# Performance work log

Hardware: AMD Instinct MI355X
Metric: run time of the kernel (lower is better)

Reference implementation:

```python
import jax, jax.numpy as jnp
import numpy as np

DIM = 192
NUM_HEADS = 6
WS = (7, 7, 7)
N_TOK = WS[0] * WS[1] * WS[2]  # 343
TABLE_SIZE = (2 * WS[0] - 1) * (2 * WS[1] - 1) * (2 * WS[2] - 1)  # 2197


def _relative_position_index():
    # faithful replication of the torch buffer construction (incl. its strides)
    coords = np.stack(np.meshgrid(np.arange(WS[0]), np.arange(WS[1]), np.arange(WS[2]), indexing='ij'))
    flat = coords.reshape(3, -1)                     # [3, N]
    rel = flat[:, :, None] - flat[:, None, :]        # [3, N, N]
    rel = rel.transpose(1, 2, 0).astype(np.int64)    # [N, N, 3]
    rel[..., 0] += WS[0] - 1
    rel[..., 1] += WS[1] - 1
    rel[..., 2] += WS[2] - 1
    rel[..., 0] *= 3 * WS[1] - 1  # = 20 (source uses window_size[1] here)
    rel[..., 1] *= 2 * WS[1] - 1  # = 13
    return rel.sum(-1)            # [N, N]


def setup_inputs() -> dict:
    key = jax.random.key(0)
    ks = jax.random.split(key, 10)
    B_, nW = 256, 64
    x1 = jax.random.normal(ks[0], (B_, N_TOK, DIM), dtype=jnp.float32)
    x2 = jax.random.normal(ks[1], (B_, N_TOK, DIM), dtype=jnp.float32)
    mask = jax.random.normal(ks[2], (nW, N_TOK, N_TOK), dtype=jnp.float32)
    table = 0.02 * jax.random.normal(ks[3], (TABLE_SIZE, NUM_HEADS), dtype=jnp.float32)
    s = DIM ** -0.5
    q_w = s * jax.random.normal(ks[4], (DIM, DIM), dtype=jnp.float32)
    q_b = jnp.zeros((DIM,), jnp.float32)
    kv_w = s * jax.random.normal(ks[5], (2 * DIM, DIM), dtype=jnp.float32)
    kv_b = jnp.zeros((2 * DIM,), jnp.float32)
    proj_w = s * jax.random.normal(ks[6], (DIM, DIM), dtype=jnp.float32)
    proj_b = jnp.zeros((DIM,), jnp.float32)
    rel_idx = jnp.asarray(_relative_position_index(), dtype=jnp.int32)
    return {"x1": x1, "x2": x2, "mask": mask, "table": table,
            "q_w": q_w, "q_b": q_b, "kv_w": kv_w, "kv_b": kv_b,
            "proj_w": proj_w, "proj_b": proj_b, "rel_idx": rel_idx}


def reference(x1, x2, mask, table, q_w, q_b, kv_w, kv_b, proj_w, proj_b, rel_idx):
    B_, N, C = x1.shape
    H = NUM_HEADS
    hd = C // H
    scale = hd ** -0.5
    # q from x1, k/v from x2 (isfusion cross-attention path)
    q = (x1 @ q_w.T + q_b).reshape(B_, N, H, hd).transpose(0, 2, 1, 3) * scale  # [B,H,N,hd]
    kv = (x2 @ kv_w.T + kv_b).reshape(B_, N, 2, H, hd).transpose(2, 0, 3, 1, 4)  # [2,B,H,N,hd]
    k, v = kv[0], kv[1]
    attn = jnp.einsum('bhnd,bhmd->bhnm', q, k)  # [B,H,N,N]
    # relative position bias gather -> [H,N,N]
    bias = table[rel_idx.reshape(-1)].reshape(N, N, H).transpose(2, 0, 1)
    attn = attn + bias[None]
    # shifted-window mask add
    nW = mask.shape[0]
    attn = (attn.reshape(B_ // nW, nW, H, N, N) + mask[None, :, None]).reshape(B_, H, N, N)
    attn = jax.nn.softmax(attn, axis=-1)
    out = jnp.einsum('bhnm,bhmd->bnhd', attn, v).reshape(B_, N, C)
    return out @ proj_w.T + proj_b
```

## Files before the change

kernel.cpp:

```cpp
#include <hip/hip_runtime.h>

typedef __attribute__((ext_vector_type(8))) short short8;
typedef __attribute__((ext_vector_type(4))) float f32x4;
typedef __attribute__((ext_vector_type(16))) float f32x16;
typedef __attribute__((ext_vector_type(4))) unsigned short us4;
typedef __attribute__((ext_vector_type(2))) unsigned int u32x2;

#define NTOK 343
#define BMP 352
#define LOG2E 1.4426950408889634f
#define FPLANE 11264
#define WPITCH 200

#define OFF_QG   0u
#define OFF_KG   33718272u
#define OFF_VT   68321280u
#define OFF_AO   102924288u
#define OFF_WB   136642560u

__device__ __forceinline__ unsigned short f2bf(float f) {
  union { float f; unsigned u; } v; v.f = f;
  unsigned r = v.u + 0x7FFFu + ((v.u >> 16) & 1u);
  return (unsigned short)(r >> 16);
}

__device__ __forceinline__ float bf2f(unsigned short b) {
  union { unsigned u; float f; } v; v.u = ((unsigned)b) << 16;
  return v.f;
}

__device__ __forceinline__ short8 ld8(const unsigned short* p) {
  return *reinterpret_cast<const short8*>(p);
}

__device__ __forceinline__ float fexp2(float x) {
  float r; asm("v_exp_f32 %0, %1" : "=v"(r) : "v"(x)); return r;
}

__device__ __forceinline__ unsigned cvtpk(float a, float b) {
  unsigned r; asm("v_cvt_pk_bf16_f32 %0, %1, %2" : "=v"(r) : "v"(a), "v"(b)); return r;
}

__device__ __forceinline__ void plswap(unsigned &a, unsigned &b) {
  asm("v_permlane32_swap_b32 %0, %1" : "+v"(a), "+v"(b));
}

__device__ __forceinline__ f32x16 mfma32(short8 a, short8 b, f32x16 c) {
  return __builtin_amdgcn_mfma_f32_32x32x16_bf16(a, b, c, 0, 0, 0);
}

__device__ __forceinline__ f32x4 mfma16(short8 a, short8 b, f32x4 c) {
  return __builtin_amdgcn_mfma_f32_16x16x32_bf16(a, b, c, 0, 0, 0);
}

union frag_u { unsigned u[4]; short8 s8; };

__device__ __forceinline__ short8 cvt8f(const float* p) {
  f32x4 a = *reinterpret_cast<const f32x4*>(p);
  f32x4 b = *reinterpret_cast<const f32x4*>(p + 4);
  frag_u f;
  f.u[0] = cvtpk(a[0], a[1]); f.u[1] = cvtpk(a[2], a[3]);
  f.u[2] = cvtpk(b[0], b[1]); f.u[3] = cvtpk(b[2], b[3]);
  return f.s8;
}

__global__ __launch_bounds__(256) void precompute(
    const float* __restrict__ mask, const float* __restrict__ table,
    const int* __restrict__ rel_idx,
    const float* __restrict__ qw, const float* __restrict__ kvw, const float* __restrict__ pw,
    unsigned short* __restrict__ wq_bf, unsigned short* __restrict__ wkv_bf,
    unsigned short* __restrict__ wp_bf,
    unsigned short* __restrict__ bias_bf, unsigned short* __restrict__ mask_bf,
    unsigned short* __restrict__ v_frag)
{
  const int idx = blockIdx.x * 256 + threadIdx.x;
  if (idx < 36864) {
    const int wi = idx;
    const float* src; unsigned short* dst; int i;
    if (wi < 9216)       { src = qw;  dst = wq_bf;  i = wi; }
    else if (wi < 27648) { src = kvw; dst = wkv_bf; i = wi - 9216; }
    else                 { src = pw;  dst = wp_bf;  i = wi - 27648; }
    f32x4 v = *reinterpret_cast<const f32x4*>(src + i * 4);
    us4 o; o[0] = f2bf(v[0]); o[1] = f2bf(v[1]); o[2] = f2bf(v[2]); o[3] = f2bf(v[3]);
    *reinterpret_cast<us4*>(dst + i * 4) = o;
  } else if (idx < 1968640) {
    const int mi = idx - 36864;
    const int row = mi / 88, q = mi - row * 88;
    const int j0 = q * 4;
    unsigned short* dst = mask_bf + row * BMP + j0;
    if (q < 85) {
      const float* src = mask + row * NTOK + j0;
      us4 o; o[0] = f2bf(LOG2E * src[0]); o[1] = f2bf(LOG2E * src[1]);
      o[2] = f2bf(LOG2E * src[2]); o[3] = f2bf(LOG2E * src[3]);
      *reinterpret_cast<us4*>(dst) = o;
    } else {
      us4 o;
      #pragma unroll
      for (int i = 0; i < 4; ++i) {
        const int col = j0 + i;
        o[i] = (col < NTOK) ? f2bf(LOG2E * mask[row * NTOK + col]) : (unsigned short)0;
      }
      *reinterpret_cast<us4*>(dst) = o;
    }
  } else if (idx < 2086289) {
    const int i = idx - 1968640;
    const int ri = rel_idx[i] * 6;
    const int rrow = i / NTOK, j = i - rrow * NTOK;
    unsigned short* dst = bias_bf + rrow * BMP + j;
    #pragma unroll
    for (int h = 0; h < 6; ++h) dst[h * (NTOK * BMP)] = f2bf(LOG2E * table[ri + h]);
  } else if (idx < 2088347) {
    const int p = idx - 2086289;
    unsigned short* dst = bias_bf + p * BMP + NTOK;
    #pragma unroll
    for (int c = 0; c < 9; ++c) dst[c] = 0;
  } else if (idx < 2284955) {
    const int i = idx - 2088347;
    const int bh = i >> 7, c = i & 127;
    short8 z = (short8){0,0,0,0,0,0,0,0};
    *reinterpret_cast<short8*>(v_frag + bh * FPLANE + 10240 + c * 8) = z;
  }
}

__global__ __launch_bounds__(256) void proj(
    const float* __restrict__ x1f, const float* __restrict__ x2f,
    const unsigned short* __restrict__ wq_bf, const unsigned short* __restrict__ wkv_bf,
    const float* __restrict__ qb, const float* __restrict__ kvb,
    unsigned short* __restrict__ q_g, unsigned short* __restrict__ k_g,
    unsigned short* __restrict__ v_frag)
{
  __shared__ __align__(16) unsigned short wLds[192 * WPITCH];

  const int tid = threadIdx.x;
  const int wv = tid >> 6, lane = tid & 63, lg = lane >> 4, lr = lane & 15;
  const int path = blockIdx.y;
  const int b = blockIdx.x & 255, seg = blockIdx.x >> 8;
  const int n0 = seg * 128 + wv * 32;

  const float* X = (path == 0) ? x1f : x2f;
  const unsigned short* Wsrc = (path == 0) ? wq_bf : (path == 1 ? wkv_bf : wkv_bf + 36864);

  #pragma unroll
  for (int i = 0; i < 18; ++i) {
    const int c = i * 256 + tid;
    const int row = c / 24, c8 = c - row * 24;
    *reinterpret_cast<short8*>(&wLds[row * WPITCH + c8 * 8]) = ld8(Wsrc + row * 192 + c8 * 8);
  }
  __syncthreads();

  const int rowbase = b * NTOK;
  const int nA = n0 + lr, nB = n0 + 16 + lr;
  const float* xr0 = X + (rowbase + (nA < NTOK ? nA : NTOK - 1)) * 192 + lg * 8;
  const float* xr1 = X + (rowbase + (nB < NTOK ? nB : NTOK - 1)) * 192 + lg * 8;

  short8 ax[2][6];
  #pragma unroll
  for (int kk = 0; kk < 6; ++kk) {
    ax[0][kk] = cvt8f(xr0 + kk * 32);
    ax[1][kk] = cvt8f(xr1 + kk * 32);
  }

  f32x4 acc[2][12];
  #pragma unroll
  for (int i = 0; i < 2; ++i)
    #pragma unroll
    for (int j = 0; j < 12; ++j) acc[i][j] = (f32x4){0.f, 0.f, 0.f, 0.f};

  if (path < 2) {
    #pragma unroll
    for (int kk = 0; kk < 6; ++kk) {
      const int k0 = kk * 32 + lg * 8;
      #pragma unroll
      for (int ct = 0; ct < 12; ++ct) {
        const short8 wf = *reinterpret_cast<const short8*>(&wLds[(ct * 16 + lr) * WPITCH + k0]);
        acc[0][ct] = mfma16(wf, ax[0][kk], acc[0][ct]);
        acc[1][ct] = mfma16(wf, ax[1][kk], acc[1][ct]);
      }
    }
    if (path == 0) {
      const float qs = 0.17677669529663687f * LOG2E;
      #pragma unroll
      for (int tt = 0; tt < 2; ++tt) {
        const int n = n0 + tt * 16 + lr;
        if (n < NTOK) {
          unsigned short* ob = q_g + (b * 6 * NTOK + n) * 32;
          #pragma unroll
          for (int ct = 0; ct < 12; ++ct) {
            const f32x4 bb = *reinterpret_cast<const f32x4*>(qb + ct * 16 + lg * 4);
            u32x2 pk;
            pk[0] = cvtpk((acc[tt][ct][0] + bb[0]) * qs, (acc[tt][ct][1] + bb[1]) * qs);
            pk[1] = cvtpk((acc[tt][ct][2] + bb[2]) * qs, (acc[tt][ct][3] + bb[3]) * qs);
            *reinterpret_cast<u32x2*>(ob + (ct >> 1) * (NTOK * 32) + (ct & 1) * 16 + lg * 4) = pk;
          }
        }
      }
    } else {
      #pragma unroll
      for (int tt = 0; tt < 2; ++tt) {
        const int n = n0 + tt * 16 + lr;
        if (n < 352) {
          unsigned short* ob = k_g + b * 6 * FPLANE + (n >> 5) * 1024
                               + ((lg >> 1) * 32 + (n & 31)) * 8 + (lg & 1) * 4;
          #pragma unroll
          for (int ct = 0; ct < 12; ++ct) {
            const f32x4 bb = *reinterpret_cast<const f32x4*>(kvb + ct * 16 + lg * 4);
            u32x2 pk;
            pk[0] = cvtpk(acc[tt][ct][0] + bb[0], acc[tt][ct][1] + bb[1]);
            pk[1] = cvtpk(acc[tt][ct][2] + bb[2], acc[tt][ct][3] + bb[3]);
            *reinterpret_cast<u32x2*>(ob + (ct >> 1) * FPLANE + (ct & 1) * 512) = pk;
          }
        }
      }
    }
  } else {
    #pragma unroll
    for (int kk = 0; kk < 6; ++kk) {
      const int k0 = kk * 32 + lg * 8;
      #pragma unroll
      for (int ct = 0; ct < 12; ++ct) {
        const short8 wf = *reinterpret_cast<const short8*>(&wLds[(ct * 16 + lr) * WPITCH + k0]);
        acc[0][ct] = mfma16(ax[0][kk], wf, acc[0][ct]);
        acc[1][ct] = mfma16(ax[1][kk], wf, acc[1][ct]);
      }
    }
    float bs[12];
    #pragma unroll
    for (int ct = 0; ct < 12; ++ct) bs[ct] = kvb[192 + ct * 16 + lr];
    #pragma unroll
    for (int tt = 0; tt < 2; ++tt) {
      const int nb = n0 + tt * 16 + lg * 4;
      if (nb < 352) {
        unsigned short* vb = v_frag + b * 6 * FPLANE + (nb >> 5) * 1024
                             + ((nb >> 4) & 1) * 512 + ((nb >> 3) & 1) * 256 + (nb & 7);
        #pragma unroll
        for (int ct = 0; ct < 12; ++ct) {
          const int d = (ct & 1) * 16 + lr;
          u32x2 pk;
          pk[0] = cvtpk(acc[tt][ct][0] + bs[ct], acc[tt][ct][1] + bs[ct]);
          pk[1] = cvtpk(acc[tt][ct][2] + bs[ct], acc[tt][ct][3] + bs[ct]);
          *reinterpret_cast<u32x2*>(vb + (ct >> 1) * FPLANE + d * 8) = pk;
        }
      }
    }
  }
}

__global__ __launch_bounds__(256, 3) void attn(
    const unsigned short* __restrict__ q_g, const unsigned short* __restrict__ k_g,
    const unsigned short* __restrict__ v_frag, const unsigned short* __restrict__ bias_bf,
    const unsigned short* __restrict__ mask_bf, unsigned short* __restrict__ attn_out)
{
  __shared__ __align__(16) unsigned short kvlds[2][FPLANE];

  const int tid = threadIdx.x;
  const int wv = tid >> 6, lane = tid & 63;
  const int l31 = lane & 31, hi = lane >> 5;
  const int s0 = blockIdx.x;
  const int xcd = s0 & 7, ii = s0 >> 3;
  const int g = xcd * 48 + (ii >> 2), mem = ii & 3;
  const int h = g >> 6, w = g & 63;
  const int b = mem * 64 + w;
  const int bid = b * 6 + h;

  const unsigned short* qp = q_g + bid * (NTOK * 32);
  const unsigned short* kpf = k_g + bid * FPLANE;
  const unsigned short* vpf = v_frag + bid * FPLANE;
  const unsigned short* bias_h = bias_bf + h * (NTOK * BMP);
  const unsigned short* mask_w = mask_bf + w * (NTOK * BMP);

  #pragma unroll
  for (int j = 0; j < 6; ++j) {
    const int c = j * 256 + tid;
    if (c < 1408) {
      *reinterpret_cast<short8*>(&kvlds[0][c * 8]) = ld8(kpf + c * 8);
      *reinterpret_cast<short8*>(&kvlds[1][c * 8]) = ld8(vpf + c * 8);
    }
  }
  __syncthreads();

  for (int qt = wv; qt < 11; qt += 4) {
    const int qq = qt * 32 + l31;
    const int qrc = qq < NTOK ? qq : NTOK - 1;
    const short8 qf0 = ld8(qp + qrc * 32 + hi * 8);
    const short8 qf1 = ld8(qp + qrc * 32 + 16 + hi * 8);
    const unsigned short* bmb = bias_h + qrc * BMP + hi * 4;
    const unsigned short* bmm = mask_w + qrc * BMP + hi * 4;

    f32x16 O;
    #pragma unroll
    for (int r = 0; r < 16; ++r) O[r] = 0.f;
    f32x4 sacc = (f32x4){0.f, 0.f, 0.f, 0.f};

    us4 nb[4], nm[4];
    #pragma unroll
    for (int gg = 0; gg < 4; ++gg) {
      nb[gg] = *reinterpret_cast<const us4*>(bmb + gg * 8);
      nm[gg] = *reinterpret_cast<const us4*>(bmm + gg * 8);
    }

    #pragma unroll
    for (int kt = 0; kt < 11; ++kt) {
      us4 cb[4], cm[4];
      #pragma unroll
      for (int gg = 0; gg < 4; ++gg) { cb[gg] = nb[gg]; cm[gg] = nm[gg]; }
      if (kt < 10) {
        const int kn = (kt + 1) * 32;
        #pragma unroll
        for (int gg = 0; gg < 4; ++gg) {
          nb[gg] = *reinterpret_cast<const us4*>(bmb + kn + gg * 8);
          nm[gg] = *reinterpret_cast<const us4*>(bmm + kn + gg * 8);
        }
      }

      const short8 kf0 = ld8(&kvlds[0][kt * 1024 + lane * 8]);
      const short8 kf1 = ld8(&kvlds[0][kt * 1024 + 512 + lane * 8]);
      f32x16 sv;
      #pragma unroll
      for (int r = 0; r < 16; ++r) sv[r] = 0.f;
      __builtin_amdgcn_s_setprio(1);
      sv = mfma32(kf0, qf0, sv);
      sv = mfma32(kf1, qf1, sv);
      __builtin_amdgcn_s_setprio(0);

      float p[16];
      #pragma unroll
      for (int gg = 0; gg < 4; ++gg) {
        #pragma unroll
        for (int j = 0; j < 4; ++j) {
          float v = sv[gg * 4 + j] + (bf2f(cb[gg][j]) + bf2f(cm[gg][j]));
          if (kt == 10 && (gg * 8 + hi * 4 + j) >= 23) v = -3.0e38f;
          p[gg * 4 + j] = fexp2(v);
        }
      }
      #pragma unroll
      for (int j = 0; j < 4; ++j)
        sacc[j] += (p[j] + p[4 + j]) + (p[8 + j] + p[12 + j]);

      unsigned c01 = cvtpk(p[0], p[1]),   c23 = cvtpk(p[2], p[3]);
      unsigned c45 = cvtpk(p[4], p[5]),   c67 = cvtpk(p[6], p[7]);
      unsigned d01 = cvtpk(p[8], p[9]),   d23 = cvtpk(p[10], p[11]);
      unsigned d45 = cvtpk(p[12], p[13]), d67 = cvtpk(p[14], p[15]);
      plswap(c01, c45); plswap(c23, c67);
      plswap(d01, d45); plswap(d23, d67);
      frag_u P0, P1;
      P0.u[0] = c01; P0.u[1] = c23; P0.u[2] = c45; P0.u[3] = c67;
      P1.u[0] = d01; P1.u[1] = d23; P1.u[2] = d45; P1.u[3] = d67;

      const short8 vf0 = ld8(&kvlds[1][kt * 1024 + lane * 8]);
      const short8 vf1 = ld8(&kvlds[1][kt * 1024 + 512 + lane * 8]);
      __builtin_amdgcn_s_setprio(1);
      O = mfma32(vf0, P0.s8, O);
      O = mfma32(vf1, P1.s8, O);
      __builtin_amdgcn_s_setprio(0);
    }

    float sum = (sacc[0] + sacc[1]) + (sacc[2] + sacc[3]);
    sum += __shfl_xor(sum, 32);
    const float inv = 1.0f / sum;
    if (qq < NTOK) {
      unsigned short* op = attn_out + (b * NTOK + qq) * 192 + h * 32;
      #pragma unroll
      for (int gg = 0; gg < 4; ++gg) {
        us4 ov;
        #pragma unroll
        for (int j = 0; j < 4; ++j) ov[j] = f2bf(O[gg * 4 + j] * inv);
        *reinterpret_cast<us4*>(op + gg * 8 + hi * 4) = ov;
      }
    }
  }
}

__global__ __launch_bounds__(256) void proj_out(
    const unsigned short* __restrict__ a_in, const unsigned short* __restrict__ wp_bf,
    const float* __restrict__ pb, float* __restrict__ out)
{
  __shared__ __align__(16) unsigned short wLds[192 * WPITCH];

  const int tid = threadIdx.x;
  const int wv = tid >> 6, lane = tid & 63, lg = lane >> 4, lr = lane & 15;
  const int t0 = blockIdx.x * 128 + wv * 32;

  #pragma unroll
  for (int i = 0; i < 18; ++i) {
    const int c = i * 256 + tid;
    const int row = c / 24, c8 = c - row * 24;
    *reinterpret_cast<short8*>(&wLds[row * WPITCH + c8 * 8]) = ld8(wp_bf + row * 192 + c8 * 8);
  }
  __syncthreads();

  const unsigned short* xr0 = a_in + (t0 + lr) * 192 + lg * 8;
  const unsigned short* xr1 = xr0 + 16 * 192;

  short8 ax[2][6];
  #pragma unroll
  for (int kk = 0; kk < 6; ++kk) {
    ax[0][kk] = ld8(xr0 + kk * 32);
    ax[1][kk] = ld8(xr1 + kk * 32);
  }

  f32x4 acc[2][12];
  #pragma unroll
  for (int i = 0; i < 2; ++i)
    #pragma unroll
    for (int j = 0; j < 12; ++j) acc[i][j] = (f32x4){0.f, 0.f, 0.f, 0.f};

  #pragma unroll
  for (int kk = 0; kk < 6; ++kk) {
    const int k0 = kk * 32 + lg * 8;
    #pragma unroll
    for (int ct = 0; ct < 12; ++ct) {
      const short8 wf = *reinterpret_cast<const short8*>(&wLds[(ct * 16 + lr) * WPITCH + k0]);
      acc[0][ct] = mfma16(wf, ax[0][kk], acc[0][ct]);
      acc[1][ct] = mfma16(wf, ax[1][kk], acc[1][ct]);
    }
  }

  #pragma unroll
  for (int tt = 0; tt < 2; ++tt) {
    const int t = t0 + tt * 16 + lr;
    float* op = out + t * 192 + lg * 4;
    #pragma unroll
    for (int ct = 0; ct < 12; ++ct) {
      const f32x4 bb = *reinterpret_cast<const f32x4*>(pb + ct * 16 + lg * 4);
      f32x4 ov;
      #pragma unroll
      for (int r = 0; r < 4; ++r) ov[r] = acc[tt][ct][r] + bb[r];
      *reinterpret_cast<f32x4*>(op + ct * 16) = ov;
    }
  }
}

extern "C" void kernel_launch(void* const* d_in, const int* in_sizes, int n_in,
                              void* d_out, int out_size, void* d_ws, size_t ws_size,
                              hipStream_t stream) {
  const float* x1    = (const float*)d_in[0];
  const float* x2    = (const float*)d_in[1];
  const float* mask  = (const float*)d_in[2];
  const float* table = (const float*)d_in[3];
  const float* qw    = (const float*)d_in[4];
  const float* qb    = (const float*)d_in[5];
  const float* kvw   = (const float*)d_in[6];
  const float* kvb   = (const float*)d_in[7];
  const float* pw    = (const float*)d_in[8];
  const float* pb    = (const float*)d_in[9];
  const int* rel_idx = (const int*)d_in[10];

  char* ws = (char*)d_ws;
  char* outc = (char*)d_out;
  unsigned short* q_g     = (unsigned short*)(ws + OFF_QG);
  unsigned short* k_g     = (unsigned short*)(ws + OFF_KG);
  unsigned short* v_frag  = (unsigned short*)(ws + OFF_VT);
  unsigned short* a_o     = (unsigned short*)(ws + OFF_AO);
  unsigned short* wq_bf   = (unsigned short*)(ws + OFF_WB);
  unsigned short* wkv_bf  = wq_bf + 36864;
  unsigned short* wp_bf   = wkv_bf + 73728;
  unsigned short* bias_bf = (unsigned short*)(outc + 33718272);
  unsigned short* mask_bf = (unsigned short*)(outc + 35167104);

  hipLaunchKernelGGL(precompute, dim3(8926), dim3(256), 0, stream,
                     mask, table, rel_idx, qw, kvw, pw,
                     wq_bf, wkv_bf, wp_bf, bias_bf, mask_bf, v_frag);
  hipLaunchKernelGGL(proj, dim3(768, 3), dim3(256), 0, stream,
                     x1, x2, wq_bf, wkv_bf, qb, kvb, q_g, k_g, v_frag);
  hipLaunchKernelGGL(attn, dim3(1536), dim3(256), 0, stream,
                     q_g, k_g, v_frag, bias_bf, mask_bf, a_o);
  hipLaunchKernelGGL(proj_out, dim3(686), dim3(256), 0, stream,
                     a_o, wp_bf, pb, (float*)d_out);
}
```

Before: 218.5 us.

## Use 512-thread attention blocks and store bias/mask in fp32

The attention kernel now runs 8 waves per block instead of 4. Each wave handles at most two of the 11 query tiles, which shortens the longest per-wave path. The precomputed relative-position bias and window mask are stored as fp32 instead of bf16, which removes the bf16-to-fp32 unpacking in the inner loop. The trade-off is twice the bias/mask memory traffic and more register pressure under launch_bounds(512,4), and the 11 tiles now spread unevenly across the 8 waves.

```diff
diff --git a/kernel.cpp b/kernel.cpp
--- a/kernel.cpp
+++ b/kernel.cpp
@@ -22,11 +22,6 @@
   union { float f; unsigned u; } v; v.f = f;
   unsigned r = v.u + 0x7FFFu + ((v.u >> 16) & 1u);
   return (unsigned short)(r >> 16);
-}
-
-__device__ __forceinline__ float bf2f(unsigned short b) {
-  union { unsigned u; float f; } v; v.u = ((unsigned)b) << 16;
-  return v.f;
 }
 
 __device__ __forceinline__ short8 ld8(const unsigned short* p) {
@@ -70,7 +65,7 @@
     const float* __restrict__ qw, const float* __restrict__ kvw, const float* __restrict__ pw,
     unsigned short* __restrict__ wq_bf, unsigned short* __restrict__ wkv_bf,
     unsigned short* __restrict__ wp_bf,
-    unsigned short* __restrict__ bias_bf, unsigned short* __restrict__ mask_bf,
+    float* __restrict__ bias_f, float* __restrict__ mask_f,
     unsigned short* __restrict__ v_frag)
 {
   const int idx = blockIdx.x * 256 + threadIdx.x;
@@ -87,33 +82,33 @@
     const int mi = idx - 36864;
     const int row = mi / 88, q = mi - row * 88;
     const int j0 = q * 4;
-    unsigned short* dst = mask_bf + row * BMP + j0;
+    float* dst = mask_f + row * BMP + j0;
     if (q < 85) {
       const float* src = mask + row * NTOK + j0;
-      us4 o; o[0] = f2bf(LOG2E * src[0]); o[1] = f2bf(LOG2E * src[1]);
-      o[2] = f2bf(LOG2E * src[2]); o[3] = f2bf(LOG2E * src[3]);
-      *reinterpret_cast<us4*>(dst) = o;
+      f32x4 o; o[0] = LOG2E * src[0]; o[1] = LOG2E * src[1];
+      o[2] = LOG2E * src[2]; o[3] = LOG2E * src[3];
+      *reinterpret_cast<f32x4*>(dst) = o;
     } else {
-      us4 o;
+      f32x4 o;
       #pragma unroll
       for (int i = 0; i < 4; ++i) {
         const int col = j0 + i;
-        o[i] = (col < NTOK) ? f2bf(LOG2E * mask[row * NTOK + col]) : (unsigned short)0;
-      }
-      *reinterpret_cast<us4*>(dst) = o;
+        o[i] = (col < NTOK) ? (LOG2E * mask[row * NTOK + col]) : 0.f;
+      }
+      *reinterpret_cast<f32x4*>(dst) = o;
     }
   } else if (idx < 2086289) {
     const int i = idx - 1968640;
     const int ri = rel_idx[i] * 6;
     const int rrow = i / NTOK, j = i - rrow * NTOK;
-    unsigned short* dst = bias_bf + rrow * BMP + j;
-    #pragma unroll
-    for (int h = 0; h < 6; ++h) dst[h * (NTOK * BMP)] = f2bf(LOG2E * table[ri + h]);
+    float* dst = bias_f + rrow * BMP + j;
+    #pragma unroll
+    for (int h = 0; h < 6; ++h) dst[h * (NTOK * BMP)] = LOG2E * table[ri + h];
   } else if (idx < 2088347) {
     const int p = idx - 2086289;
-    unsigned short* dst = bias_bf + p * BMP + NTOK;
-    #pragma unroll
-    for (int c = 0; c < 9; ++c) dst[c] = 0;
+    float* dst = bias_f + p * BMP + NTOK;
+    #pragma unroll
+    for (int c = 0; c < 9; ++c) dst[c] = 0.f;
   } else if (idx < 2284955) {
     const int i = idx - 2088347;
     const int bh = i >> 7, c = i & 127;
@@ -245,10 +240,10 @@
   }
 }
 
-__global__ __launch_bounds__(256, 3) void attn(
+__global__ __launch_bounds__(512, 4) void attn(
     const unsigned short* __restrict__ q_g, const unsigned short* __restrict__ k_g,
-    const unsigned short* __restrict__ v_frag, const unsigned short* __restrict__ bias_bf,
-    const unsigned short* __restrict__ mask_bf, unsigned short* __restrict__ attn_out)
+    const unsigned short* __restrict__ v_frag, const float* __restrict__ bias_f,
+    const float* __restrict__ mask_f, unsigned short* __restrict__ attn_out)
 {
   __shared__ __align__(16) unsigned short kvlds[2][FPLANE];
 
@@ -265,12 +260,12 @@
   const unsigned short* qp = q_g + bid * (NTOK * 32);
   const unsigned short* kpf = k_g + bid * FPLANE;
   const unsigned short* vpf = v_frag + bid * FPLANE;
-  const unsigned short* bias_h = bias_bf + h * (NTOK * BMP);
-  const unsigned short* mask_w = mask_bf + w * (NTOK * BMP);
-
-  #pragma unroll
-  for (int j = 0; j < 6; ++j) {
-    const int c = j * 256 + tid;
+  const float* bias_h = bias_f + h * (NTOK * BMP);
+  const float* mask_w = mask_f + w * (NTOK * BMP);
+
+  #pragma unroll
+  for (int j = 0; j < 3; ++j) {
+    const int c = j * 512 + tid;
     if (c < 1408) {
       *reinterpret_cast<short8*>(&kvlds[0][c * 8]) = ld8(kpf + c * 8);
       *reinterpret_cast<short8*>(&kvlds[1][c * 8]) = ld8(vpf + c * 8);
@@ -278,37 +273,37 @@
   }
   __syncthreads();
 
-  for (int qt = wv; qt < 11; qt += 4) {
+  for (int qt = wv; qt < 11; qt += 8) {
     const int qq = qt * 32 + l31;
     const int qrc = qq < NTOK ? qq : NTOK - 1;
     const short8 qf0 = ld8(qp + qrc * 32 + hi * 8);
     const short8 qf1 = ld8(qp + qrc * 32 + 16 + hi * 8);
-    const unsigned short* bmb = bias_h + qrc * BMP + hi * 4;
-    const unsigned short* bmm = mask_w + qrc * BMP + hi * 4;
+    const float* bmb = bias_h + qrc * BMP + hi * 4;
+    const float* bmm = mask_w + qrc * BMP + hi * 4;
 
     f32x16 O;
     #pragma unroll
     for (int r = 0; r < 16; ++r) O[r] = 0.f;
     f32x4 sacc = (f32x4){0.f, 0.f, 0.f, 0.f};
 
-    us4 nb[4], nm[4];
+    f32x4 nb[4], nm[4];
     #pragma unroll
     for (int gg = 0; gg < 4; ++gg) {
-      nb[gg] = *reinterpret_cast<const us4*>(bmb + gg * 8);
-      nm[gg] = *reinterpret_cast<const us4*>(bmm + gg * 8);
+      nb[gg] = *reinterpret_cast<const f32x4*>(bmb + gg * 8);
+      nm[gg] = *reinterpret_cast<const f32x4*>(bmm + gg * 8);
     }
 
     #pragma unroll
     for (int kt = 0; kt < 11; ++kt) {
-      us4 cb[4], cm[4];
+      f32x4 cb[4], cm[4];
       #pragma unroll
       for (int gg = 0; gg < 4; ++gg) { cb[gg] = nb[gg]; cm[gg] = nm[gg]; }
       if (kt < 10) {
         const int kn = (kt + 1) * 32;
         #pragma unroll
         for (int gg = 0; gg < 4; ++gg) {
-          nb[gg] = *reinterpret_cast<const us4*>(bmb + kn + gg * 8);
-          nm[gg] = *reinterpret_cast<const us4*>(bmm + kn + gg * 8);
+          nb[gg] = *reinterpret_cast<const f32x4*>(bmb + kn + gg * 8);
+          nm[gg] = *reinterpret_cast<const f32x4*>(bmm + kn + gg * 8);
         }
       }
 
@@ -327,7 +322,7 @@
       for (int gg = 0; gg < 4; ++gg) {
         #pragma unroll
         for (int j = 0; j < 4; ++j) {
-          float v = sv[gg * 4 + j] + (bf2f(cb[gg][j]) + bf2f(cm[gg][j]));
+          float v = sv[gg * 4 + j] + (cb[gg][j] + cm[gg][j]);
           if (kt == 10 && (gg * 8 + hi * 4 + j) >= 23) v = -3.0e38f;
           p[gg * 4 + j] = fexp2(v);
         }
@@ -454,16 +449,16 @@
   unsigned short* wq_bf   = (unsigned short*)(ws + OFF_WB);
   unsigned short* wkv_bf  = wq_bf + 36864;
   unsigned short* wp_bf   = wkv_bf + 73728;
-  unsigned short* bias_bf = (unsigned short*)(outc + 33718272);
-  unsigned short* mask_bf = (unsigned short*)(outc + 35167104);
+  float* bias_f           = (float*)outc;
+  float* mask_f           = (float*)(outc + 2897664);
 
   hipLaunchKernelGGL(precompute, dim3(8926), dim3(256), 0, stream,
                      mask, table, rel_idx, qw, kvw, pw,
-                     wq_bf, wkv_bf, wp_bf, bias_bf, mask_bf, v_frag);
+                     wq_bf, wkv_bf, wp_bf, bias_f, mask_f, v_frag);
   hipLaunchKernelGGL(proj, dim3(768, 3), dim3(256), 0, stream,
                      x1, x2, wq_bf, wkv_bf, qb, kvb, q_g, k_g, v_frag);
-  hipLaunchKernelGGL(attn, dim3(1536), dim3(256), 0, stream,
-                     q_g, k_g, v_frag, bias_bf, mask_bf, a_o);
+  hipLaunchKernelGGL(attn, dim3(1536), dim3(512), 0, stream,
+                     q_g, k_g, v_frag, bias_f, mask_f, a_o);
   hipLaunchKernelGGL(proj_out, dim3(686), dim3(256), 0, stream,
                      a_o, wp_bf, pb, (float*)d_out);
 }
```

Measured after the change: 301.0 us. 37.7% more time.
